# Performance work log

Measured on AMD Instinct MI355X. Metric: run time of the kernel, lower is better.

The kernel has to match this reference:

```python
import jax, jax.numpy as jnp
import numpy as np

N = 50000      # nodes
E = 800000     # edges (avg degree 16)
F_IN = 128     # input feature dim
HID = 64       # hidden_channels
HEADS = 2
NEG_SLOPE = 0.2


def setup_inputs() -> dict:
    key = jax.random.key(0)
    ks = jax.random.split(key, 20)
    w = lambda k, shape: jax.random.normal(k, shape, jnp.float32) * 0.1
    inp = {
        "x": jax.random.normal(ks[0], (N, F_IN), jnp.float32),
        "edge_index": jax.random.randint(ks[1], (2, E), 0, N, dtype=jnp.int32),
    }
    # layer specs: (in_dim, heads) ; out per head = HID
    specs = [(F_IN, HEADS), (HID * HEADS, HEADS), (HID * HEADS, HEADS), (HID * HEADS, 1)]
    ki = 2
    for i, (fin, h) in enumerate(specs, 1):
        inp[f"Wl{i}"] = w(ks[ki], (fin, h * HID)); ki += 1
        inp[f"Wr{i}"] = w(ks[ki], (fin, h * HID)); ki += 1
        inp[f"att{i}"] = w(ks[ki], (h, HID)); ki += 1
        inp[f"b{i}"] = jnp.zeros((h * HID,), jnp.float32)
    return inp


def gat_layer(x, src, dst, Wl, Wr, att, b):
    # GATv2Conv: e_ij = att . LeakyReLU(Wl x_j + Wr x_i), softmax over incoming edges of i
    H, C = att.shape
    n = x.shape[0]
    xl = (x @ Wl).reshape(n, H, C)   # source-side transform
    xr = (x @ Wr).reshape(n, H, C)   # target-side transform
    e = jax.nn.leaky_relu(xl[src] + xr[dst], negative_slope=NEG_SLOPE)  # [E,H,C]
    score = jnp.einsum('ehc,hc->eh', e, att)                            # [E,H]
    # segment softmax over destination nodes
    m = jax.ops.segment_max(score, dst, num_segments=n)
    m = jnp.where(jnp.isfinite(m), m, 0.0)  # nodes with no in-edges
    ex = jnp.exp(score - m[dst])
    den = jax.ops.segment_sum(ex, dst, num_segments=n)
    alpha = ex / (den[dst] + 1e-16)                                     # [E,H]
    out = jax.ops.segment_sum(xl[src] * alpha[:, :, None], dst, num_segments=n)  # [N,H,C]
    return out.reshape(n, H * C) + b


def reference(x, edge_index, Wl1, Wr1, att1, b1, Wl2, Wr2, att2, b2,
              Wl3, Wr3, att3, b3, Wl4, Wr4, att4, b4):
    src, dst = edge_index[0], edge_index[1]
    x = jax.nn.relu(gat_layer(x, src, dst, Wl1, Wr1, att1, b1))
    x = jax.nn.relu(gat_layer(x, src, dst, Wl2, Wr2, att2, b2))
    x = jax.nn.relu(gat_layer(x, src, dst, Wl3, Wr3, att3, b3))
    return gat_layer(x, src, dst, Wl4, Wr4, att4, b4)  # [N, HID]
```

## Files before the change

### kernel.cpp

```cpp
#include <hip/hip_runtime.h>
#include <hip/hip_fp16.h>
#include <math.h>
#include <limits.h>

#define FIN 128
#define NEG_SLOPE 0.2f

typedef _Float16 f16x8 __attribute__((ext_vector_type(8)));
typedef float f32x4 __attribute__((ext_vector_type(4)));
typedef float f32x2 __attribute__((ext_vector_type(2)));

static __device__ __forceinline__ f32x2 pk_add(f32x2 a, f32x2 b) {
    f32x2 d; asm("v_pk_add_f32 %0, %1, %2" : "=v"(d) : "v"(a), "v"(b)); return d;
}
static __device__ __forceinline__ f32x2 pk_fma(f32x2 a, f32x2 b, f32x2 c) {
    f32x2 d; asm("v_pk_fma_f32 %0, %1, %2, %3" : "=v"(d) : "v"(a), "v"(b), "v"(c)); return d;
}

static __device__ __forceinline__ f32x2 h2f2x(unsigned int u) {
    __half2 h = *reinterpret_cast<__half2*>(&u);
    float2 f = __half22float2(h);
    return (f32x2){f.x, f.y};
}

template <int CTRL>
static __device__ __forceinline__ float dpp_add(float x) {
    int t = __builtin_amdgcn_update_dpp(0, __builtin_bit_cast(int, x), CTRL, 0xF, 0xF, true);
    return x + __builtin_bit_cast(float, t);
}
static __device__ __forceinline__ float reduce8_dpp(float p) {
    p = dpp_add<0xB1>(p);
    p = dpp_add<0x4E>(p);
    p = dpp_add<0x141>(p);
    return p;
}


__global__ void k_hist_part(const int* __restrict__ dst, int* __restrict__ counts,
                            int E, int span) {
    const int r = blockIdx.x & 7;
    const int chunk = blockIdx.x >> 3;
    const int nchunks = gridDim.x >> 3;
    const int lo = r * span, hi = lo + span;
    const int per = (E + nchunks - 1) / nchunks;
    const int e1 = min(E, (chunk + 1) * per);
    for (int e = chunk * per + threadIdx.x; e < e1; e += blockDim.x) {
        int d = dst[e];
        if (d >= lo && d < hi) atomicAdd(&counts[d], 1);
    }
}

__global__ void k_scatter_part(const int* __restrict__ dst, const int* __restrict__ rowptr,
                               int* __restrict__ nfill, int* __restrict__ colids,
                               int E, int span) {
    const int r = blockIdx.x & 7;
    const int chunk = blockIdx.x >> 3;
    const int nchunks = gridDim.x >> 3;
    const int lo = r * span, hi = lo + span;
    const int per = (E + nchunks - 1) / nchunks;
    const int e1 = min(E, (chunk + 1) * per);
    for (int e = chunk * per + threadIdx.x; e < e1; e += blockDim.x) {
        int d = dst[e];
        if (d >= lo && d < hi) {
            int pos = atomicAdd(&nfill[d], 1);
            colids[rowptr[d] + pos] = e;
        }
    }
}

__global__ void k_scan1(const int* __restrict__ counts, int* __restrict__ incl,
                        int* __restrict__ partial, int n) {
    __shared__ int tmp[1024];
    int tid = threadIdx.x, base = blockIdx.x * 1024;
    int v = (base + tid < n) ? counts[base + tid] : 0;
    tmp[tid] = v;
    __syncthreads();
    for (int off = 1; off < 1024; off <<= 1) {
        int t = (tid >= off) ? tmp[tid - off] : 0;
        __syncthreads();
        tmp[tid] += t;
        __syncthreads();
    }
    if (base + tid < n) incl[base + tid] = tmp[tid];
    if (tid == 1023) partial[blockIdx.x] = tmp[1023];
}

__global__ void k_scan3(const int* __restrict__ counts, const int* __restrict__ incl,
                        const int* __restrict__ partial, int* __restrict__ rowptr,
                        int* __restrict__ nfill, int n, int nb) {
    __shared__ int sbase;
    if (threadIdx.x == 0) {
        int b = 0;
        for (int p = 0; p < (int)blockIdx.x; ++p) b += partial[p];
        sbase = b;
        if ((int)blockIdx.x == nb - 1) {
            int tot = b;
            for (int p = blockIdx.x; p < nb; ++p) tot += partial[p];
            rowptr[n] = tot;
        }
    }
    __syncthreads();
    int i = blockIdx.x * 1024 + threadIdx.x;
    if (i < n) {
        rowptr[i] = sbase + incl[i] - counts[i];
        nfill[i] = 0;
    }
}

__global__ void k_sort(const int* __restrict__ rowptr, const int* __restrict__ colids,
                       const int* __restrict__ esrc, int* __restrict__ colsrc, int n) {
    int node = blockIdx.x * 4 + (threadIdx.x >> 6);
    int lane = threadIdx.x & 63;
    if (node >= n) return;
    int s = rowptr[node], e = rowptr[node + 1];
    int d = e - s;
    if (d <= 0) return;
    if (d <= 64) {
        int v = (lane < d) ? colids[s + lane] : INT_MAX;
        int rank = 0;
        for (int j = 0; j < d; ++j) {
            int vj = __shfl(v, j, 64);
            rank += (vj < v) ? 1 : 0;
        }
        if (lane < d) colsrc[s + rank] = esrc[v];
    } else {
        if (lane == 0) {
            int last = -1;
            for (int k = 0; k < d; ++k) {
                int best = INT_MAX;
                for (int j = s; j < e; ++j) {
                    int id = colids[j];
                    if (id > last && id < best) best = id;
                }
                colsrc[s + k] = esrc[best];
                last = best;
            }
        }
    }
}


struct WprepArgs {
    const float* Wl[4];
    const float* Wr[4];
    __half* Wz[4];
};

__global__ void k_wprep_all(WprepArgs a) {
    int b = blockIdx.x;
    int layer = (b < 16) ? 0 : (b < 32) ? 1 : (b < 48) ? 2 : 3;
    int base = layer * 16;
    int HC = (layer == 3) ? 64 : 128;
    int NT = 2 * HC / 16;
    int tid = (b - base) * 256 + threadIdx.x;
    int l = tid & 63, c = tid >> 6;
    int ks = c / NT, nt = c % NT;
    int col = nt * 16 + (l & 15);
    int kbase = ks * 32 + ((l >> 4) << 3);
    const float* W = (col < HC) ? (a.Wl[layer] + col) : (a.Wr[layer] + (col - HC));
    __half h[8];
#pragma unroll
    for (int j = 0; j < 8; ++j) h[j] = __float2half(W[(size_t)(kbase + j) * HC]);
    *(uint4*)&a.Wz[layer][(size_t)tid * 8] = *(const uint4*)h;
}


template <int HC, bool CVT>
__global__ void __launch_bounds__(256) k_gemm_mfma(
        const void* __restrict__ Ain, const __half* __restrict__ Wz,
        __half* __restrict__ xl, float* __restrict__ xr, int n) {
    constexpr int NT = 2 * HC / 16;
    const int l = threadIdx.x & 63;
    const int wid = threadIdx.x >> 6;
    const int r0 = (blockIdx.x * 4 + wid) * 16;
    if (r0 >= n) return;
    const int m = l & 15, kb = l >> 4;
    const int ra = min(r0 + m, n - 1);
    const f16x8* Bz = (const f16x8*)Wz;

    f32x4 acc[NT];
#pragma unroll
    for (int nt = 0; nt < NT; ++nt) acc[nt] = (f32x4){0.f, 0.f, 0.f, 0.f};

#pragma unroll
    for (int ks = 0; ks < 4; ++ks) {
        f16x8 a;
        if (CVT) {
            const float* Af = (const float*)Ain + (size_t)ra * FIN + kb * 8 + ks * 32;
            float4 f0 = *(const float4*)Af;
            float4 f1 = *(const float4*)(Af + 4);
            a[0] = (_Float16)f0.x; a[1] = (_Float16)f0.y;
            a[2] = (_Float16)f0.z; a[3] = (_Float16)f0.w;
            a[4] = (_Float16)f1.x; a[5] = (_Float16)f1.y;
            a[6] = (_Float16)f1.z; a[7] = (_Float16)f1.w;
        } else {
            a = *(const f16x8*)((const _Float16*)Ain + (size_t)ra * FIN + kb * 8 + ks * 32);
        }
#pragma unroll
        for (int nt = 0; nt < NT; ++nt) {
            f16x8 b = Bz[(ks * NT + nt) * 64 + l];
            acc[nt] = __builtin_amdgcn_mfma_f32_16x16x32_f16(a, b, acc[nt], 0, 0, 0);
        }
    }

    const int rb = r0 + kb * 4;
#pragma unroll
    for (int nt = 0; nt < NT; ++nt) {
        int c = nt * 16 + m;
        if (nt < NT / 2) {
#pragma unroll
            for (int r = 0; r < 4; ++r) {
                int row = rb + r;
                if (row < n) xl[(size_t)row * HC + c] = __float2half(acc[nt][r]);
            }
        } else {
            int cd = c - HC;
#pragma unroll
            for (int r = 0; r < 4; ++r) {
                int row = rb + r;
                if (row < n) xr[(size_t)row * HC + cd] = acc[nt][r];
            }
        }
    }
}


template <bool RELU>
__global__ void __launch_bounds__(256) k_fused2(
        const __half* __restrict__ xlh, const float* __restrict__ xr,
        const int* __restrict__ rowptr, const int* __restrict__ colsrc,
        const float* __restrict__ attc, const float* __restrict__ bias,
        __half* __restrict__ out, int N) {
    const int lane = threadIdx.x & 63;
    const int g = lane >> 4;
    const int s = lane & 15;
    const int c0 = s * 8;
    int i = blockIdx.x * 4 + (threadIdx.x >> 6);
    const int stride = gridDim.x * 4;
    const float L2E = 1.4426950408889634f;

    f32x2 a6[4], a4[4];
    {
        float4 a0 = *(const float4*)&attc[c0];
        float4 a1 = *(const float4*)&attc[c0 + 4];
        float t[8] = {a0.x, a0.y, a0.z, a0.w, a1.x, a1.y, a1.z, a1.w};
#pragma unroll
        for (int k = 0; k < 4; ++k) {
            a6[k] = (f32x2){0.6f * L2E * t[2 * k], 0.6f * L2E * t[2 * k + 1]};
            a4[k] = (f32x2){0.4f * L2E * t[2 * k], 0.4f * L2E * t[2 * k + 1]};
        }
    }

    for (; i < N; i += stride) {
        f32x2 xrv[4];
        {
            float4 r0 = *(const float4*)&xr[(size_t)i * 128 + c0];
            float4 r1 = *(const float4*)&xr[(size_t)i * 128 + c0 + 4];
            xrv[0] = (f32x2){r0.x, r0.y}; xrv[1] = (f32x2){r0.z, r0.w};
            xrv[2] = (f32x2){r1.x, r1.y}; xrv[3] = (f32x2){r1.z, r1.w};
        }
        const int st = rowptr[i], en = rowptr[i + 1];
        float den = 0.f;
        f32x2 acc[4];
#pragma unroll
        for (int k = 0; k < 4; ++k) acc[k] = (f32x2){0.f, 0.f};

        if (st < en) {
            uint4 w0 = *(const uint4*)(xlh + ((size_t)colsrc[st + g] << 7) + c0);
            uint4 w1 = *(const uint4*)(xlh + ((size_t)colsrc[st + 4 + g] << 7) + c0);
            uint4 w2 = *(const uint4*)(xlh + ((size_t)colsrc[st + 8 + g] << 7) + c0);
            uint4 w3 = *(const uint4*)(xlh + ((size_t)colsrc[st + 12 + g] << 7) + c0);
            int i0 = colsrc[st + 16 + g];
            int i1 = colsrc[st + 20 + g];
            for (int j = st; j < en; j += 8) {
                uint4 n0 = *(const uint4*)(xlh + ((size_t)i0 << 7) + c0);
                uint4 n1 = *(const uint4*)(xlh + ((size_t)i1 << 7) + c0);
                i0 = colsrc[j + 24 + g];
                i1 = colsrc[j + 28 + g];

#pragma unroll
                for (int q = 0; q < 2; ++q) {
                    const uint4 w = q ? w1 : w0;
                    f32x2 xv[4];
                    xv[0] = h2f2x(w.x); xv[1] = h2f2x(w.y);
                    xv[2] = h2f2x(w.z); xv[3] = h2f2x(w.w);
                    f32x2 sc = (f32x2){0.f, 0.f};
#pragma unroll
                    for (int k = 0; k < 4; ++k) {
                        f32x2 u = pk_add(xv[k], xrv[k]);
                        sc = pk_fma(u, a6[k], sc);
                        f32x2 ua = {__builtin_fabsf(u.x), __builtin_fabsf(u.y)};
                        sc = pk_fma(ua, a4[k], sc);
                    }
                    float p = reduce8_dpp(sc.x + sc.y);
                    p = (j + q * 4 + g < en) ? p : -INFINITY;
                    float pe = exp2f(p);
                    den += pe;
                    f32x2 pe2 = (f32x2){pe, pe};
#pragma unroll
                    for (int k = 0; k < 4; ++k) acc[k] = pk_fma(pe2, xv[k], acc[k]);
                }
                w0 = w2; w1 = w3; w2 = n0; w3 = n1;
            }
        }

#pragma unroll
        for (int off = 16; off <= 32; off <<= 1) {
            den += __shfl_xor(den, off, 64);
#pragma unroll
            for (int k = 0; k < 4; ++k) {
                acc[k].x += __shfl_xor(acc[k].x, off, 64);
                acc[k].y += __shfl_xor(acc[k].y, off, 64);
            }
        }

        if (g == 0) {
            float4 b0 = *(const float4*)&bias[c0];
            float4 b1 = *(const float4*)&bias[c0 + 4];
            float bv[8] = {b0.x, b0.y, b0.z, b0.w, b1.x, b1.y, b1.z, b1.w};
            float inv = 1.f / (den + 1e-16f);
            __half hb[8];
#pragma unroll
            for (int k = 0; k < 8; ++k) {
                float av = (k & 1) ? acc[k >> 1].y : acc[k >> 1].x;
                float o = fmaf(av, inv, bv[k]);
                if (RELU) o = fmaxf(o, 0.f);
                hb[k] = __float2half(o);
            }
            *(uint4*)&out[(size_t)i * 128 + c0] = *(const uint4*)hb;
        }
    }
}


__global__ void __launch_bounds__(256) k_fused1(
        const __half* __restrict__ xlh, const float* __restrict__ xr,
        const int* __restrict__ rowptr, const int* __restrict__ colsrc,
        const float* __restrict__ attc, const float* __restrict__ bias,
        float* __restrict__ out, int N) {
    const int lane = threadIdx.x & 63;
    const int g = lane >> 3;
    const int s = lane & 7;
    const int c0 = s * 8;
    int i = blockIdx.x * 4 + (threadIdx.x >> 6);
    const int stride = gridDim.x * 4;
    const float L2E = 1.4426950408889634f;

    f32x2 a6[4], a4[4];
    {
        float4 a0 = *(const float4*)&attc[c0];
        float4 a1 = *(const float4*)&attc[c0 + 4];
        float t[8] = {a0.x, a0.y, a0.z, a0.w, a1.x, a1.y, a1.z, a1.w};
#pragma unroll
        for (int k = 0; k < 4; ++k) {
            a6[k] = (f32x2){0.6f * L2E * t[2 * k], 0.6f * L2E * t[2 * k + 1]};
            a4[k] = (f32x2){0.4f * L2E * t[2 * k], 0.4f * L2E * t[2 * k + 1]};
        }
    }

    for (; i < N; i += stride) {
        f32x2 xrv[4];
        {
            float4 r0 = *(const float4*)&xr[(size_t)i * 64 + c0];
            float4 r1 = *(const float4*)&xr[(size_t)i * 64 + c0 + 4];
            xrv[0] = (f32x2){r0.x, r0.y}; xrv[1] = (f32x2){r0.z, r0.w};
            xrv[2] = (f32x2){r1.x, r1.y}; xrv[3] = (f32x2){r1.z, r1.w};
        }
        const int st = rowptr[i], en = rowptr[i + 1];
        float den = 0.f;
        f32x2 acc[4];
#pragma unroll
        for (int k = 0; k < 4; ++k) acc[k] = (f32x2){0.f, 0.f};

        if (st < en) {
            uint4 w0 = *(const uint4*)(xlh + ((size_t)colsrc[st + g] << 6) + c0);
            uint4 w1 = *(const uint4*)(xlh + ((size_t)colsrc[st + 8 + g] << 6) + c0);
            int i0 = colsrc[st + 16 + g];
            int i1 = colsrc[st + 24 + g];
            for (int j = st; j < en; j += 16) {
                uint4 n0 = *(const uint4*)(xlh + ((size_t)i0 << 6) + c0);
                uint4 n1 = *(const uint4*)(xlh + ((size_t)i1 << 6) + c0);
                i0 = colsrc[j + 32 + g];
                i1 = colsrc[j + 40 + g];

#pragma unroll
                for (int q = 0; q < 2; ++q) {
                    const uint4 w = q ? w1 : w0;
                    f32x2 xv[4];
                    xv[0] = h2f2x(w.x); xv[1] = h2f2x(w.y);
                    xv[2] = h2f2x(w.z); xv[3] = h2f2x(w.w);
                    f32x2 sc = (f32x2){0.f, 0.f};
#pragma unroll
                    for (int k = 0; k < 4; ++k) {
                        f32x2 u = pk_add(xv[k], xrv[k]);
                        sc = pk_fma(u, a6[k], sc);
                        f32x2 ua = {__builtin_fabsf(u.x), __builtin_fabsf(u.y)};
                        sc = pk_fma(ua, a4[k], sc);
                    }
                    float p = reduce8_dpp(sc.x + sc.y);
                    p = (j + q * 8 + g < en) ? p : -INFINITY;
                    float pe = exp2f(p);
                    den += pe;
                    f32x2 pe2 = (f32x2){pe, pe};
#pragma unroll
                    for (int k = 0; k < 4; ++k) acc[k] = pk_fma(pe2, xv[k], acc[k]);
                }
                w0 = n0; w1 = n1;
            }
        }

#pragma unroll
        for (int off = 8; off <= 32; off <<= 1) {
            den += __shfl_xor(den, off, 64);
#pragma unroll
            for (int k = 0; k < 4; ++k) {
                acc[k].x += __shfl_xor(acc[k].x, off, 64);
                acc[k].y += __shfl_xor(acc[k].y, off, 64);
            }
        }

        if (g == 0) {
            float4 b0 = *(const float4*)&bias[c0];
            float4 b1 = *(const float4*)&bias[c0 + 4];
            float bv[8] = {b0.x, b0.y, b0.z, b0.w, b1.x, b1.y, b1.z, b1.w};
            float inv = 1.f / (den + 1e-16f);
            float o[8];
#pragma unroll
            for (int k = 0; k < 8; ++k) {
                float av = (k & 1) ? acc[k >> 1].y : acc[k >> 1].x;
                o[k] = fmaf(av, inv, bv[k]);
            }
            *(float4*)&out[(size_t)i * 64 + c0] = make_float4(o[0], o[1], o[2], o[3]);
            *(float4*)&out[(size_t)i * 64 + c0 + 4] = make_float4(o[4], o[5], o[6], o[7]);
        }
    }
}


static inline size_t align_up(size_t v, size_t a) { return (v + a - 1) & ~(a - 1); }

extern "C" void kernel_launch(void* const* d_in, const int* in_sizes, int n_in,
                              void* d_out, int out_size, void* d_ws, size_t ws_size,
                              hipStream_t stream) {
    const float* x = (const float*)d_in[0];
    const int* ei = (const int*)d_in[1];
    const int N = in_sizes[0] / FIN;
    const int E = in_sizes[1] / 2;
    const int* esrc = ei;
    const int* edst = ei + E;

    const float* Wl1 = (const float*)d_in[2];
    const float* Wr1 = (const float*)d_in[3];
    const float* att1 = (const float*)d_in[4];
    const float* b1 = (const float*)d_in[5];
    const float* Wl2 = (const float*)d_in[6];
    const float* Wr2 = (const float*)d_in[7];
    const float* att2 = (const float*)d_in[8];
    const float* b2 = (const float*)d_in[9];
    const float* Wl3 = (const float*)d_in[10];
    const float* Wr3 = (const float*)d_in[11];
    const float* att3 = (const float*)d_in[12];
    const float* b3 = (const float*)d_in[13];
    const float* Wl4 = (const float*)d_in[14];
    const float* Wr4 = (const float*)d_in[15];
    const float* att4 = (const float*)d_in[16];
    const float* b4 = (const float*)d_in[17];

    const int nb = (N + 1023) / 1024;
    const int span = (N + 7) / 8;

    size_t off = 0;
    char* w = (char*)d_ws;
    auto alloc = [&](size_t bytes) {
        char* p = w + off;
        off = align_up(off + bytes, 256);
        return p;
    };
    int* rowptr = (int*)alloc((size_t)(N + 1) * 4);
    int* nfill = (int*)alloc((size_t)N * 4);
    int* incl = (int*)alloc((size_t)N * 4);
    int* partial = (int*)alloc(1024 * 4);
    int* colids = (int*)alloc((size_t)E * 4);
    int* colsrc = (int*)alloc((size_t)(E + 64) * 4);
    __half* xb16 = (__half*)alloc((size_t)N * FIN * 2);
    __half* xlh = (__half*)alloc((size_t)N * FIN * 2);
    float* xr = (float*)alloc((size_t)N * FIN * 4);
    __half* Wz1 = (__half*)alloc(65536);
    __half* Wz2 = (__half*)alloc(65536);
    __half* Wz3 = (__half*)alloc(65536);
    __half* Wz4 = (__half*)alloc(32768);
    if (off > ws_size) return;

    hipMemsetAsync(nfill, 0, (size_t)N * 4, stream);
    hipMemsetAsync(colsrc + E, 0, 64 * 4, stream);
    k_hist_part<<<2048, 256, 0, stream>>>(edst, nfill, E, span);
    k_scan1<<<nb, 1024, 0, stream>>>(nfill, incl, partial, N);
    k_scan3<<<nb, 1024, 0, stream>>>(nfill, incl, partial, rowptr, nfill, N, nb);
    k_scatter_part<<<2048, 256, 0, stream>>>(edst, rowptr, nfill, colids, E, span);
    k_sort<<<(N + 3) / 4, 256, 0, stream>>>(rowptr, colids, esrc, colsrc, N);

    WprepArgs wa;
    wa.Wl[0] = Wl1; wa.Wl[1] = Wl2; wa.Wl[2] = Wl3; wa.Wl[3] = Wl4;
    wa.Wr[0] = Wr1; wa.Wr[1] = Wr2; wa.Wr[2] = Wr3; wa.Wr[3] = Wr4;
    wa.Wz[0] = Wz1; wa.Wz[1] = Wz2; wa.Wz[2] = Wz3; wa.Wz[3] = Wz4;
    k_wprep_all<<<56, 256, 0, stream>>>(wa);

    const int gg = (N + 63) / 64;
    const int gf = (N + 3) / 4;

    k_gemm_mfma<128, true><<<gg, 256, 0, stream>>>(x, Wz1, xlh, xr, N);
    k_fused2<true><<<gf, 256, 0, stream>>>(xlh, xr, rowptr, colsrc, att1, b1, xb16, N);
    k_gemm_mfma<128, false><<<gg, 256, 0, stream>>>(xb16, Wz2, xlh, xr, N);
    k_fused2<true><<<gf, 256, 0, stream>>>(xlh, xr, rowptr, colsrc, att2, b2, xb16, N);
    k_gemm_mfma<128, false><<<gg, 256, 0, stream>>>(xb16, Wz3, xlh, xr, N);
    k_fused2<true><<<gf, 256, 0, stream>>>(xlh, xr, rowptr, colsrc, att3, b3, xb16, N);
    k_gemm_mfma<64, false><<<gg, 256, 0, stream>>>(xb16, Wz4, xlh, xr, N);
    k_fused1<<<gf, 256, 0, stream>>>(xlh, xr, rowptr, colsrc, att4, b4, (float*)d_out, N);
}
```

Baseline: 385.5 us.

## Prefetch next node's row pointers and neighbor indices in persistent aggregation loop

The fused attention-aggregation kernels become persistent, launching a fixed grid of 2048 blocks instead of one wave per node. Each wave loads the next node's rowptr range and first neighbor indices while it processes the current node, which hides the dependent index-load latency between nodes. The cost is fewer resident waves when the per-node work is small, and extra live registers. It also drops the empty-row guard, so it now relies on padded colsrc reads being safe.

Result: no change. 380.4 us (-1.3%).

```diff
diff --git a/kernel.cpp b/kernel.cpp
--- a/kernel.cpp
+++ b/kernel.cpp
@@ -251,7 +251,23 @@
         }
     }
 
-    for (; i < N; i += stride) {
+    if (i >= N) return;
+    int st = rowptr[i];
+    int en = rowptr[i + 1];
+    int c0i = colsrc[st + g];
+    int c1i = colsrc[st + 4 + g];
+    int c2i = colsrc[st + 8 + g];
+    int c3i = colsrc[st + 12 + g];
+    int p0 = colsrc[st + 16 + g];
+    int p1 = colsrc[st + 20 + g];
+
+    while (true) {
+        const int inext = i + stride;
+        int nst = 0, nen = 0;
+        if (inext < N) {
+            nst = rowptr[inext];
+            nen = rowptr[inext + 1];
+        }
         f32x2 xrv[4];
         {
             float4 r0 = *(const float4*)&xr[(size_t)i * 128 + c0];
@@ -259,49 +275,55 @@
             xrv[0] = (f32x2){r0.x, r0.y}; xrv[1] = (f32x2){r0.z, r0.w};
             xrv[2] = (f32x2){r1.x, r1.y}; xrv[3] = (f32x2){r1.z, r1.w};
         }
-        const int st = rowptr[i], en = rowptr[i + 1];
+        uint4 w0 = *(const uint4*)(xlh + ((size_t)c0i << 7) + c0);
+        uint4 w1 = *(const uint4*)(xlh + ((size_t)c1i << 7) + c0);
+        uint4 w2 = *(const uint4*)(xlh + ((size_t)c2i << 7) + c0);
+        uint4 w3 = *(const uint4*)(xlh + ((size_t)c3i << 7) + c0);
+        int i0 = p0, i1 = p1;
+
         float den = 0.f;
         f32x2 acc[4];
 #pragma unroll
         for (int k = 0; k < 4; ++k) acc[k] = (f32x2){0.f, 0.f};
 
-        if (st < en) {
-            uint4 w0 = *(const uint4*)(xlh + ((size_t)colsrc[st + g] << 7) + c0);
-            uint4 w1 = *(const uint4*)(xlh + ((size_t)colsrc[st + 4 + g] << 7) + c0);
-            uint4 w2 = *(const uint4*)(xlh + ((size_t)colsrc[st + 8 + g] << 7) + c0);
-            uint4 w3 = *(const uint4*)(xlh + ((size_t)colsrc[st + 12 + g] << 7) + c0);
-            int i0 = colsrc[st + 16 + g];
-            int i1 = colsrc[st + 20 + g];
-            for (int j = st; j < en; j += 8) {
-                uint4 n0 = *(const uint4*)(xlh + ((size_t)i0 << 7) + c0);
-                uint4 n1 = *(const uint4*)(xlh + ((size_t)i1 << 7) + c0);
-                i0 = colsrc[j + 24 + g];
-                i1 = colsrc[j + 28 + g];
-
-#pragma unroll
-                for (int q = 0; q < 2; ++q) {
-                    const uint4 w = q ? w1 : w0;
-                    f32x2 xv[4];
-                    xv[0] = h2f2x(w.x); xv[1] = h2f2x(w.y);
-                    xv[2] = h2f2x(w.z); xv[3] = h2f2x(w.w);
-                    f32x2 sc = (f32x2){0.f, 0.f};
-#pragma unroll
-                    for (int k = 0; k < 4; ++k) {
-                        f32x2 u = pk_add(xv[k], xrv[k]);
-                        sc = pk_fma(u, a6[k], sc);
-                        f32x2 ua = {__builtin_fabsf(u.x), __builtin_fabsf(u.y)};
-                        sc = pk_fma(ua, a4[k], sc);
-                    }
-                    float p = reduce8_dpp(sc.x + sc.y);
-                    p = (j + q * 4 + g < en) ? p : -INFINITY;
-                    float pe = exp2f(p);
-                    den += pe;
-                    f32x2 pe2 = (f32x2){pe, pe};
-#pragma unroll
-                    for (int k = 0; k < 4; ++k) acc[k] = pk_fma(pe2, xv[k], acc[k]);
+        for (int j = st; j < en; j += 8) {
+            uint4 n0 = *(const uint4*)(xlh + ((size_t)i0 << 7) + c0);
+            uint4 n1 = *(const uint4*)(xlh + ((size_t)i1 << 7) + c0);
+            i0 = colsrc[j + 24 + g];
+            i1 = colsrc[j + 28 + g];
+
+#pragma unroll
+            for (int q = 0; q < 2; ++q) {
+                const uint4 w = q ? w1 : w0;
+                f32x2 xv[4];
+                xv[0] = h2f2x(w.x); xv[1] = h2f2x(w.y);
+                xv[2] = h2f2x(w.z); xv[3] = h2f2x(w.w);
+                f32x2 sc = (f32x2){0.f, 0.f};
+#pragma unroll
+                for (int k = 0; k < 4; ++k) {
+                    f32x2 u = pk_add(xv[k], xrv[k]);
+                    sc = pk_fma(u, a6[k], sc);
+                    f32x2 ua = {__builtin_fabsf(u.x), __builtin_fabsf(u.y)};
+                    sc = pk_fma(ua, a4[k], sc);
                 }
-                w0 = w2; w1 = w3; w2 = n0; w3 = n1;
-            }
+                float p = reduce8_dpp(sc.x + sc.y);
+                p = (j + q * 4 + g < en) ? p : -INFINITY;
+                float pe = exp2f(p);
+                den += pe;
+                f32x2 pe2 = (f32x2){pe, pe};
+#pragma unroll
+                for (int k = 0; k < 4; ++k) acc[k] = pk_fma(pe2, xv[k], acc[k]);
+            }
+            w0 = w2; w1 = w3; w2 = n0; w3 = n1;
+        }
+
+        if (inext < N) {
+            c0i = colsrc[nst + g];
+            c1i = colsrc[nst + 4 + g];
+            c2i = colsrc[nst + 8 + g];
+            c3i = colsrc[nst + 12 + g];
+            p0 = colsrc[nst + 16 + g];
+            p1 = colsrc[nst + 20 + g];
         }
 
 #pragma unroll
@@ -329,6 +351,9 @@
             }
             *(uint4*)&out[(size_t)i * 128 + c0] = *(const uint4*)hb;
         }
+
+        if (inext >= N) break;
+        i = inext; st = nst; en = nen;
     }
 }
 
@@ -358,7 +383,21 @@
         }
     }
 
-    for (; i < N; i += stride) {
+    if (i >= N) return;
+    int st = rowptr[i];
+    int en = rowptr[i + 1];
+    int c0i = colsrc[st + g];
+    int c1i = colsrc[st + 8 + g];
+    int p0 = colsrc[st + 16 + g];
+    int p1 = colsrc[st + 24 + g];
+
+    while (true) {
+        const int inext = i + stride;
+        int nst = 0, nen = 0;
+        if (inext < N) {
+            nst = rowptr[inext];
+            nen = rowptr[inext + 1];
+        }
         f32x2 xrv[4];
         {
             float4 r0 = *(const float4*)&xr[(size_t)i * 64 + c0];
@@ -366,47 +405,51 @@
             xrv[0] = (f32x2){r0.x, r0.y}; xrv[1] = (f32x2){r0.z, r0.w};
             xrv[2] = (f32x2){r1.x, r1.y}; xrv[3] = (f32x2){r1.z, r1.w};
         }
-        const int st = rowptr[i], en = rowptr[i + 1];
+        uint4 w0 = *(const uint4*)(xlh + ((size_t)c0i << 6) + c0);
+        uint4 w1 = *(const uint4*)(xlh + ((size_t)c1i << 6) + c0);
+        int i0 = p0, i1 = p1;
+
         float den = 0.f;
         f32x2 acc[4];
 #pragma unroll
         for (int k = 0; k < 4; ++k) acc[k] = (f32x2){0.f, 0.f};
 
-        if (st < en) {
-            uint4 w0 = *(const uint4*)(xlh + ((size_t)colsrc[st + g] << 6) + c0);
-            uint4 w1 = *(const uint4*)(xlh + ((size_t)colsrc[st + 8 + g] << 6) + c0);
-            int i0 = colsrc[st + 16 + g];
-            int i1 = colsrc[st + 24 + g];
-            for (int j = st; j < en; j += 16) {
-                uint4 n0 = *(const uint4*)(xlh + ((size_t)i0 << 6) + c0);
-                uint4 n1 = *(const uint4*)(xlh + ((size_t)i1 << 6) + c0);
-                i0 = colsrc[j + 32 + g];
-                i1 = colsrc[j + 40 + g];
-
-#pragma unroll
-                for (int q = 0; q < 2; ++q) {
-                    const uint4 w = q ? w1 : w0;
-                    f32x2 xv[4];
-                    xv[0] = h2f2x(w.x); xv[1] = h2f2x(w.y);
-                    xv[2] = h2f2x(w.z); xv[3] = h2f2x(w.w);
-                    f32x2 sc = (f32x2){0.f, 0.f};
-#pragma unroll
-                    for (int k = 0; k < 4; ++k) {
-                        f32x2 u = pk_add(xv[k], xrv[k]);
-                        sc = pk_fma(u, a6[k], sc);
-                        f32x2 ua = {__builtin_fabsf(u.x), __builtin_fabsf(u.y)};
-                        sc = pk_fma(ua, a4[k], sc);
-                    }
-                    float p = reduce8_dpp(sc.x + sc.y);
-                    p = (j + q * 8 + g < en) ? p : -INFINITY;
-                    float pe = exp2f(p);
-                    den += pe;
-                    f32x2 pe2 = (f32x2){pe, pe};
-#pragma unroll
-                    for (int k = 0; k < 4; ++k) acc[k] = pk_fma(pe2, xv[k], acc[k]);
+        for (int j = st; j < en; j += 16) {
+            uint4 n0 = *(const uint4*)(xlh + ((size_t)i0 << 6) + c0);
+            uint4 n1 = *(const uint4*)(xlh + ((size_t)i1 << 6) + c0);
+            i0 = colsrc[j + 32 + g];
+            i1 = colsrc[j + 40 + g];
+
+#pragma unroll
+            for (int q = 0; q < 2; ++q) {
+                const uint4 w = q ? w1 : w0;
+                f32x2 xv[4];
+                xv[0] = h2f2x(w.x); xv[1] = h2f2x(w.y);
+                xv[2] = h2f2x(w.z); xv[3] = h2f2x(w.w);
+                f32x2 sc = (f32x2){0.f, 0.f};
+#pragma unroll
+                for (int k = 0; k < 4; ++k) {
+                    f32x2 u = pk_add(xv[k], xrv[k]);
+                    sc = pk_fma(u, a6[k], sc);
+                    f32x2 ua = {__builtin_fabsf(u.x), __builtin_fabsf(u.y)};
+                    sc = pk_fma(ua, a4[k], sc);
                 }
-                w0 = n0; w1 = n1;
-            }
+                float p = reduce8_dpp(sc.x + sc.y);
+                p = (j + q * 8 + g < en) ? p : -INFINITY;
+                float pe = exp2f(p);
+                den += pe;
+                f32x2 pe2 = (f32x2){pe, pe};
+#pragma unroll
+                for (int k = 0; k < 4; ++k) acc[k] = pk_fma(pe2, xv[k], acc[k]);
+            }
+            w0 = n0; w1 = n1;
+        }
+
+        if (inext < N) {
+            c0i = colsrc[nst + g];
+            c1i = colsrc[nst + 8 + g];
+            p0 = colsrc[nst + 16 + g];
+            p1 = colsrc[nst + 24 + g];
         }
 
 #pragma unroll
@@ -433,6 +476,9 @@
             *(float4*)&out[(size_t)i * 64 + c0] = make_float4(o[0], o[1], o[2], o[3]);
             *(float4*)&out[(size_t)i * 64 + c0 + 4] = make_float4(o[4], o[5], o[6], o[7]);
         }
+
+        if (inext >= N) break;
+        i = inext; st = nst; en = nen;
     }
 }
 
@@ -506,7 +552,7 @@
     k_wprep_all<<<56, 256, 0, stream>>>(wa);
 
     const int gg = (N + 63) / 64;
-    const int gf = (N + 3) / 4;
+    const int gf = 2048;
 
     k_gemm_mfma<128, true><<<gg, 256, 0, stream>>>(x, Wz1, xlh, xr, N);
     k_fused2<true><<<gf, 256, 0, stream>>>(xlh, xr, rowptr, colsrc, att1, b1, xb16, N);
```
